# Kernel tuning notes

Hardware: AMD Instinct MI355X
Metric: run time of the kernel (lower is better)

The kernel has to match this reference:

```python
import jax, jax.numpy as jnp
import numpy as np

NP_ = 20000   # paper nodes
NA_ = 20000   # author nodes
E_AP = 400000
E_PP = 400000
D_IN, D_H, HEADS, D_HEAD, D_FF, D_OUT = 128, 256, 8, 32, 2048, 64


def setup_inputs() -> dict:
    key = jax.random.key(0)
    ks = iter(jax.random.split(key, 48))
    def nrm(shape, s=0.1):
        return jax.random.normal(next(ks), shape, jnp.float32) * s
    inp = {
        'feat_paper': nrm((NP_, D_IN), 1.0),
        'feat_author': nrm((NA_, D_IN), 1.0),
        'W_in_p': nrm((D_H, D_IN)), 'b_in_p': nrm((D_H,), 0.05),
        'W_in_a': nrm((D_H, D_IN)), 'b_in_a': nrm((D_H,), 0.05),
        'W_gat_ap': nrm((D_H, D_H)), 'al_ap': nrm((HEADS, D_HEAD)), 'ar_ap': nrm((HEADS, D_HEAD)), 'b_gat_ap': nrm((D_H,), 0.05),
        'W_gat_pp': nrm((D_H, D_H)), 'al_pp': nrm((HEADS, D_HEAD)), 'ar_pp': nrm((HEADS, D_HEAD)), 'b_gat_pp': nrm((D_H,), 0.05),
        'Wqkv_s': nrm((3 * D_H, D_H)), 'bqkv_s': nrm((3 * D_H,), 0.05), 'Wo_s': nrm((D_H, D_H)), 'bo_s': nrm((D_H,), 0.05),
        'Wqkv_c': nrm((3 * D_H, D_H)), 'bqkv_c': nrm((3 * D_H,), 0.05), 'Wo_c': nrm((D_H, D_H)), 'bo_c': nrm((D_H,), 0.05),
        'W_ff1': nrm((D_FF, D_H)), 'b_ff1': nrm((D_FF,), 0.05),
        'W_ff2': nrm((D_H, D_FF)), 'b_ff2': nrm((D_H,), 0.05),
        'ln1_g': jnp.ones((D_H,), jnp.float32), 'ln1_b': jnp.zeros((D_H,), jnp.float32),
        'ln2_g': jnp.ones((D_H,), jnp.float32), 'ln2_b': jnp.zeros((D_H,), jnp.float32),
        'ln3_g': jnp.ones((D_H,), jnp.float32), 'ln3_b': jnp.zeros((D_H,), jnp.float32),
        'W_pred': nrm((D_OUT, 3 * D_H)), 'b_pred': nrm((D_OUT,), 0.05),
        'ap_src': jax.random.randint(next(ks), (E_AP,), 0, NA_),
        'ap_dst': jax.random.randint(next(ks), (E_AP,), 0, NP_),
        'pp_src': jax.random.randint(next(ks), (E_PP,), 0, NP_),
        'pp_dst': jax.random.randint(next(ks), (E_PP,), 0, NP_),
    }
    return inp


def _leaky(x):
    return jnp.where(x > 0, x, 0.2 * x)  # DGL GATConv negative_slope=0.2


def _gat(x, src, dst, W, al, ar, b):
    """DGL GATConv on homogeneous graph with self-loops appended (eval mode)."""
    N = x.shape[0]
    h = (x @ W.T).reshape(N, HEADS, D_HEAD)          # fc has no bias in GATConv
    el = (h * al[None]).sum(-1)                      # (N, H)
    er = (h * ar[None]).sum(-1)                      # (N, H)
    sl = jnp.arange(N, dtype=src.dtype)              # self loops (add_self_loop)
    s = jnp.concatenate([src, sl])
    d = jnp.concatenate([dst, sl])
    e = _leaky(el[s] + er[d])                        # (E+N, H)
    m = jax.ops.segment_max(e, d, num_segments=N)    # edge-softmax per dst
    a = jnp.exp(e - m[d])
    z = jax.ops.segment_sum(a, d, num_segments=N)
    out = jax.ops.segment_sum(a[:, :, None] * h[s], d, num_segments=N)
    out = out / z[:, :, None] + b.reshape(1, HEADS, D_HEAD)
    return out.reshape(N, D_H)                       # flatten(start_dim=1)


def _ln(x, g, b):
    mu = x.mean(-1, keepdims=True)
    v = ((x - mu) ** 2).mean(-1, keepdims=True)
    return (x - mu) / jnp.sqrt(v + 1e-5) * g + b


def _mha(xq, xkv, Wqkv, bqkv, Wo, bo):
    Wq, Wk, Wv = jnp.split(Wqkv, 3, axis=0)
    bq, bk, bv = jnp.split(bqkv, 3)
    B, S, _ = xq.shape
    Sk = xkv.shape[1]
    q = (xq @ Wq.T + bq).reshape(B, S, HEADS, D_HEAD)
    k = (xkv @ Wk.T + bk).reshape(B, Sk, HEADS, D_HEAD)
    v = (xkv @ Wv.T + bv).reshape(B, Sk, HEADS, D_HEAD)
    att = jnp.einsum('bqhd,bkhd->bhqk', q, k) * (D_HEAD ** -0.5)
    a = jax.nn.softmax(att, axis=-1)
    o = jnp.einsum('bhqk,bkhd->bqhd', a, v).reshape(B, S, D_H)
    return o @ Wo.T + bo


def reference(feat_paper, feat_author, W_in_p, b_in_p, W_in_a, b_in_a,
              W_gat_ap, al_ap, ar_ap, b_gat_ap, W_gat_pp, al_pp, ar_pp, b_gat_pp,
              Wqkv_s, bqkv_s, Wo_s, bo_s, Wqkv_c, bqkv_c, Wo_c, bo_c,
              W_ff1, b_ff1, W_ff2, b_ff2, ln1_g, ln1_b, ln2_g, ln2_b, ln3_g, ln3_b,
              W_pred, b_pred, ap_src, ap_dst, pp_src, pp_dst):
    # fc_in per node type
    hp = feat_paper @ W_in_p.T + b_in_p              # (NP, D_H)
    ha = feat_author @ W_in_a.T + b_in_a             # (NA, D_H)
    Na = ha.shape[0]
    # etype 'ap': bipartite author->paper, to_homogeneous orders [author; paper]
    x_ap = jnp.concatenate([ha, hp], axis=0)
    out_ap = _gat(x_ap, ap_src, ap_dst + Na, W_gat_ap, al_ap, ar_ap, b_gat_ap)[Na:]
    # etype 'pp': paper->paper (single node set)
    out_pp = _gat(hp, pp_src, pp_dst, W_gat_pp, al_pp, ar_pp, b_gat_pp)
    # h dict order: 'paper', 'paper-author', 'paper-paper'
    tgt = jnp.stack([hp, out_ap, out_pp], axis=1)    # (NP, 3, D_H)
    # TransformerDecoderLayer (post-norm, relu, eval): memory = tgt
    x = _ln(tgt + _mha(tgt, tgt, Wqkv_s, bqkv_s, Wo_s, bo_s), ln1_g, ln1_b)
    x = _ln(x + _mha(x, tgt, Wqkv_c, bqkv_c, Wo_c, bo_c), ln2_g, ln2_b)
    ff = jax.nn.relu(x @ W_ff1.T + b_ff1) @ W_ff2.T + b_ff2
    z = _ln(x + ff, ln3_g, ln3_b)
    return z.reshape(z.shape[0], -1) @ W_pred.T + b_pred
```

## Files before the change

kernel.cpp:

```cpp
#include <hip/hip_runtime.h>
#include <hip/hip_bf16.h>
#include <cstdint>
#include <cstddef>

#define NP_N 20000
#define NA_N 20000
#define E_AP_N 400000
#define E_PP_N 400000

typedef __attribute__((ext_vector_type(8))) short bf16x8;
typedef __attribute__((ext_vector_type(4))) float f32x4;

__device__ __forceinline__ float b2f(ushort u) { return __uint_as_float(((uint32_t)u) << 16); }
__device__ __forceinline__ ushort f2b(float f) {
    uint32_t x = __float_as_uint(f);
    return (ushort)((x + 0x7fffu + ((x >> 16) & 1u)) >> 16);
}

#define LGKM_BARRIER() do { \
    asm volatile("s_waitcnt lgkmcnt(0)" ::: "memory"); \
    __builtin_amdgcn_s_barrier(); \
    __builtin_amdgcn_sched_barrier(0); \
} while (0)

#define NJOBS 14
struct PackJobs {
    const float* src[NJOBS];
    void* dst[NJOBS];
    int M[NJOBS], K[NJOBS];
    int type[NJOBS];
    int nquad[NJOBS];
    int blk0[NJOBS];
};

__global__ void pack_all_kernel(PackJobs J)
{
    int b = blockIdx.x;
    int j = 0;
    while (j + 1 < NJOBS && b >= J.blk0[j + 1]) ++j;
    int u = (b - J.blk0[j]) * 256 + threadIdx.x;
    if (u >= J.nquad[j]) return;
    int ty = J.type[j];
    const float* src = J.src[j];
    if (ty == 3) {
        float4 v = ((const float4*)src)[u];
        ushort4 o;
        o.x = f2b(v.x); o.y = f2b(v.y); o.z = f2b(v.z); o.w = f2b(v.w);
        ((ushort4*)J.dst[j])[u] = o;
    } else if (ty == 4) {
        int4 z = {0, 0, 0, 0};
        ((int4*)J.dst[j])[u] = z;
    } else if (ty == 0) {
        int M = J.M[j], K = J.K[j];
        int KT = K >> 5;
        int q = u & 1023;
        int jt = u >> 10;
        int t = jt % KT, jj = jt / KT;
        int ks = q >> 8, rem = q & 255;
        int r = rem >> 1;
        int e0 = (rem & 1) * 4;
        int row = jj * 128 + r;
        ushort4 o = {0, 0, 0, 0};
        if (row < M) {
            const float* s = src + (size_t)row * K + t * 32 + ks * 8 + e0;
            o.x = f2b(s[0]); o.y = f2b(s[1]); o.z = f2b(s[2]); o.w = f2b(s[3]);
        }
        ((ushort4*)J.dst[j])[u] = o;
    } else if (ty == 1) {
        int q = u & 2047, chunk = u >> 11;
        int s = q >> 6, rem = q & 63;
        int fl = rem >> 1, e0 = (rem & 1) * 4;
        const float* sp = src + (size_t)(chunk * 32 + fl) * 256 + s * 8 + e0;
        ushort4 o;
        o.x = f2b(sp[0]); o.y = f2b(sp[1]); o.z = f2b(sp[2]); o.w = f2b(sp[3]);
        ((ushort4*)J.dst[j])[u] = o;
    } else {
        int q = u & 2047, chunk = u >> 11;
        int s2 = q >> 9, rem = q & 511;
        int c = rem >> 1, e0 = (rem & 1) * 4;
        const float* sp = src + (size_t)c * 2048 + chunk * 32 + s2 * 8 + e0;
        ushort4 o;
        o.x = f2b(sp[0]); o.y = f2b(sp[1]); o.z = f2b(sp[2]); o.w = f2b(sp[3]);
        ((ushort4*)J.dst[j])[u] = o;
    }
}

template <int OUT_MODE>
__global__ __launch_bounds__(256) void gemm_mfma(
    const ushort* __restrict__ A, const ushort* __restrict__ Bp,
    const float* __restrict__ bias, void* __restrict__ Cv,
    int N, int M, int K, int lda)
{
    __shared__ __align__(16) ushort Ab[3][4096];
    __shared__ __align__(16) ushort Bb[3][4096];
    const int tid = threadIdx.x;
    const int lane = tid & 63;
    const int w = tid >> 6;
    const int wr = w >> 1, wc = w & 1;
    const int row0 = blockIdx.x * 128;
    const int col0 = blockIdx.y * 128;
    const int KT = K >> 5;
    const ushort* Bbase = Bp + (size_t)blockIdx.y * KT * 4096;
    f32x4 acc[4][4] = {};

    size_t aoff[2];
#pragma unroll
    for (int i = 0; i < 2; ++i) {
        int r = row0 + i * 64 + lane;
        if (r > N - 1) r = N - 1;
        aoff[i] = (size_t)r * lda + w * 8;
    }

    auto stage = [&](int buf, int t) {
        const int k0 = t << 5;
#pragma unroll
        for (int i = 0; i < 2; ++i) {
            __builtin_amdgcn_global_load_lds(
                (const __attribute__((address_space(1))) void*)(A + aoff[i] + k0),
                (__attribute__((address_space(3))) void*)(&Ab[buf][(w * 2 + i) * 512]), 16, 0, 0);
        }
#pragma unroll
        for (int i = 0; i < 2; ++i) {
            __builtin_amdgcn_global_load_lds(
                (const __attribute__((address_space(1))) void*)(Bbase + (size_t)t * 4096 + (w * 2 + i) * 512 + lane * 8),
                (__attribute__((address_space(3))) void*)(&Bb[buf][(w * 2 + i) * 512]), 16, 0, 0);
        }
    };

    stage(0, 0);
    stage(1, 1);

    int cur = 0;
    for (int t = 0; t < KT; ++t) {
        if (t + 1 < KT) { asm volatile("s_waitcnt vmcnt(4)" ::: "memory"); }
        else            { asm volatile("s_waitcnt vmcnt(0)" ::: "memory"); }
        __builtin_amdgcn_s_barrier();
        __builtin_amdgcn_sched_barrier(0);
        if (t + 2 < KT) {
            int nb = cur - 1; if (nb < 0) nb = 2;
            stage(nb, t + 2);
        }

        bf16x8 af[4], bfr[4];
        const int ks = lane >> 4;
        const int rl = lane & 15;
#pragma unroll
        for (int m = 0; m < 4; ++m)
            af[m] = *(const bf16x8*)&Ab[cur][ks * 1024 + (wr * 64 + m * 16 + rl) * 8];
#pragma unroll
        for (int n = 0; n < 4; ++n)
            bfr[n] = *(const bf16x8*)&Bb[cur][ks * 1024 + (wc * 64 + n * 16 + rl) * 8];
#pragma unroll
        for (int m = 0; m < 4; ++m)
#pragma unroll
            for (int n = 0; n < 4; ++n)
                acc[m][n] = __builtin_amdgcn_mfma_f32_16x16x32_bf16(af[m], bfr[n], acc[m][n], 0, 0, 0);

        cur = (cur == 2) ? 0 : cur + 1;
    }

#pragma unroll
    for (int m = 0; m < 4; ++m) {
#pragma unroll
        for (int n = 0; n < 4; ++n) {
            int gc = col0 + wc * 64 + n * 16 + (lane & 15);
            if (gc >= M) continue;
            float bv = bias ? bias[gc] : 0.f;
#pragma unroll
            for (int r = 0; r < 4; ++r) {
                int grow = row0 + wr * 64 + m * 16 + (lane >> 4) * 4 + r;
                if (grow >= N) continue;
                float v = acc[m][n][r] + bv;
                if (OUT_MODE == 2) v = fmaxf(v, 0.f);
                if (OUT_MODE == 1) ((float*)Cv)[(size_t)grow * M + gc] = v;
                else ((ushort*)Cv)[(size_t)grow * M + gc] = f2b(v);
            }
        }
    }
}

static inline void gemm_bf(const ushort* A, const ushort* Bp, const float* bias, void* C,
                           int N, int M, int K, int lda, int mode, hipStream_t s)
{
    dim3 g((N + 127) / 128, (M + 127) / 128);
    if (mode == 0)      gemm_mfma<0><<<g, 256, 0, s>>>(A, Bp, bias, C, N, M, K, lda);
    else if (mode == 1) gemm_mfma<1><<<g, 256, 0, s>>>(A, Bp, bias, C, N, M, K, lda);
    else                gemm_mfma<2><<<g, 256, 0, s>>>(A, Bp, bias, C, N, M, K, lda);
}

__global__ __launch_bounds__(256, 2) void ff_ln_kernel(
    const ushort* __restrict__ W1p, const ushort* __restrict__ W2p,
    const float* __restrict__ b1, const float* __restrict__ b2,
    const float* __restrict__ g3, const float* __restrict__ be3,
    ushort* X, int N)
{
    __shared__ __align__(16) ushort W1buf[8192];
    __shared__ __align__(16) ushort W2buf[8192];
    __shared__ __align__(16) ushort Sbuf[2048];
    const int tid = threadIdx.x;
    const int lane = tid & 63;
    const int w = tid >> 6;
    const int wr = w >> 1, wc = w & 1;
    const int row0 = blockIdx.x * 64;
    const int rl = lane & 15;
    const int ks = lane >> 4;

    bf16x8 xf[2][8];
#pragma unroll
    for (int m = 0; m < 2; ++m) {
        int gr = row0 + wr * 32 + m * 16 + rl;
        if (gr > N - 1) gr = N - 1;
        const ushort* xrow = X + (size_t)gr * 256 + ks * 8;
#pragma unroll
        for (int kc = 0; kc < 8; ++kc)
            xf[m][kc] = *(const bf16x8*)(xrow + kc * 32);
    }

    f32x4 oacc[2][8] = {};

    for (int fc = 0; fc < 64; ++fc) {
#pragma unroll
        for (int i = 0; i < 8; ++i) {
            int ii = w * 8 + i;
            const ushort* src;
            ushort* dst;
            if (ii < 16) {
                src = W1p + (size_t)fc * 8192 + ii * 512 + lane * 8;
                dst = &W1buf[ii * 512];
            } else {
                src = W2p + (size_t)fc * 8192 + (ii - 16) * 512 + lane * 8;
                dst = &W2buf[(ii - 16) * 512];
            }
            __builtin_amdgcn_global_load_lds(
                (const __attribute__((address_space(1))) void*)src,
                (__attribute__((address_space(3))) void*)dst, 16, 0, 0);
        }
        __syncthreads();

        f32x4 sacc[2] = {};
#pragma unroll
        for (int kc = 0; kc < 8; ++kc) {
            bf16x8 w1f = *(const bf16x8*)&W1buf[(kc * 4 + ks) * 256 + (wc * 16 + rl) * 8];
#pragma unroll
            for (int m = 0; m < 2; ++m)
                sacc[m] = __builtin_amdgcn_mfma_f32_16x16x32_bf16(w1f, xf[m][kc], sacc[m], 0, 0, 0);
        }
        {
            const int f0 = fc * 32;
            const int fb = wc * 16 + ks * 4;
            const int sidx = wc * 2 + (ks >> 1);
            const int e0 = (ks & 1) * 4;
            float4 b1v = *(const float4*)&b1[f0 + fb];
#pragma unroll
            for (int m = 0; m < 2; ++m) {
                ushort4 o;
                o.x = f2b(fmaxf(sacc[m][0] + b1v.x, 0.f));
                o.y = f2b(fmaxf(sacc[m][1] + b1v.y, 0.f));
                o.z = f2b(fmaxf(sacc[m][2] + b1v.z, 0.f));
                o.w = f2b(fmaxf(sacc[m][3] + b1v.w, 0.f));
                *(ushort4*)&Sbuf[(sidx * 64 + wr * 32 + m * 16 + rl) * 8 + e0] = o;
            }
        }
        LGKM_BARRIER();

        {
            bf16x8 sf[2];
#pragma unroll
            for (int m = 0; m < 2; ++m)
                sf[m] = *(const bf16x8*)&Sbuf[ks * 512 + (wr * 32 + m * 16 + rl) * 8];
#pragma unroll
            for (int n = 0; n < 8; ++n) {
                bf16x8 w2f = *(const bf16x8*)&W2buf[ks * 2048 + (wc * 128 + n * 16 + rl) * 8];
#pragma unroll
                for (int m = 0; m < 2; ++m)
                    oacc[m][n] = __builtin_amdgcn_mfma_f32_16x16x32_bf16(sf[m], w2f, oacc[m][n], 0, 0, 0);
            }
        }
        __syncthreads();
    }

    float2* lnb = (float2*)W1buf;
    float psum[2][4] = {}, psq[2][4] = {};
#pragma unroll
    for (int n = 0; n < 8; ++n) {
        int c = wc * 128 + n * 16 + rl;
        float bv = b2[c];
#pragma unroll
        for (int m = 0; m < 2; ++m)
#pragma unroll
            for (int r = 0; r < 4; ++r) {
                int grow = row0 + wr * 32 + m * 16 + ks * 4 + r;
                float v = oacc[m][n][r] + bv + b2f(X[(size_t)grow * 256 + c]);
                oacc[m][n][r] = v;
                psum[m][r] += v;
                psq[m][r] = fmaf(v, v, psq[m][r]);
            }
    }
#pragma unroll
    for (int off = 8; off >= 1; off >>= 1)
#pragma unroll
        for (int m = 0; m < 2; ++m)
#pragma unroll
            for (int r = 0; r < 4; ++r) {
                psum[m][r] += __shfl_xor(psum[m][r], off);
                psq[m][r]  += __shfl_xor(psq[m][r], off);
            }
    if (rl == 0) {
#pragma unroll
        for (int m = 0; m < 2; ++m)
#pragma unroll
            for (int r = 0; r < 4; ++r) {
                int lr = wr * 32 + m * 16 + ks * 4 + r;
                lnb[wc * 64 + lr] = make_float2(psum[m][r], psq[m][r]);
            }
    }
    __syncthreads();
    float mean_[2][4], rstd_[2][4];
#pragma unroll
    for (int m = 0; m < 2; ++m)
#pragma unroll
        for (int r = 0; r < 4; ++r) {
            int lr = wr * 32 + m * 16 + ks * 4 + r;
            float2 a0 = lnb[lr], a1 = lnb[64 + lr];
            float mean = (a0.x + a1.x) * (1.f / 256.f);
            float var = (a0.y + a1.y) * (1.f / 256.f) - mean * mean;
            mean_[m][r] = mean;
            rstd_[m][r] = rsqrtf(var + 1e-5f);
        }
#pragma unroll
    for (int n = 0; n < 8; ++n) {
        int c = wc * 128 + n * 16 + rl;
        float gv = g3[c], bev = be3[c];
#pragma unroll
        for (int m = 0; m < 2; ++m)
#pragma unroll
            for (int r = 0; r < 4; ++r) {
                int grow = row0 + wr * 32 + m * 16 + ks * 4 + r;
                if (grow < N)
                    X[(size_t)grow * 256 + c] =
                        f2b((oacc[m][n][r] - mean_[m][r]) * rstd_[m][r] * gv + bev);
            }
    }
}

__global__ void copy_col0_kernel(const ushort* __restrict__ src, ushort* __restrict__ tgt, int n)
{
    int i = blockIdx.x * blockDim.x + threadIdx.x;
    if (i >= n) return;
    int p = i >> 6, c = i & 63;
    ((ushort4*)tgt)[(size_t)p * 192 + c] = ((const ushort4*)src)[(size_t)p * 64 + c];
}

__global__ void attn_lr_all_kernel(
    const ushort* __restrict__ h0, const float* __restrict__ al0, const float* __restrict__ ar0,
    float* __restrict__ el0, float* __restrict__ er0,
    const ushort* __restrict__ h1, const float* __restrict__ al1, const float* __restrict__ ar1,
    float* __restrict__ el1, float* __restrict__ er1)
{
    int idx = blockIdx.x * blockDim.x + threadIdx.x;
    if (idx >= 480000) return;
    const ushort* h; const float *a1, *a2; float *el, *er; int i;
    if (idx < 320000) { h = h0; a1 = al0; a2 = ar0; el = el0; er = er0; i = idx; }
    else { h = h1; a1 = al1; a2 = ar1; el = el1; er = er1; i = idx - 320000; }
    int hd = i & 7;
    const ushort* hp = h + (size_t)(i >> 3) * 256 + hd * 32;
    const float* p1 = a1 + hd * 32;
    const float* p2 = a2 + hd * 32;
    float s1 = 0.f, s2 = 0.f;
#pragma unroll
    for (int j = 0; j < 8; ++j) {
        ushort4 t = ((const ushort4*)hp)[j];
        float v0 = b2f(t.x), v1 = b2f(t.y), v2 = b2f(t.z), v3 = b2f(t.w);
        s1 = fmaf(v0, p1[j * 4 + 0], s1); s2 = fmaf(v0, p2[j * 4 + 0], s2);
        s1 = fmaf(v1, p1[j * 4 + 1], s1); s2 = fmaf(v1, p2[j * 4 + 1], s2);
        s1 = fmaf(v2, p1[j * 4 + 2], s1); s2 = fmaf(v2, p2[j * 4 + 2], s2);
        s1 = fmaf(v3, p1[j * 4 + 3], s1); s2 = fmaf(v3, p2[j * 4 + 3], s2);
    }
    el[i] = s1;
    er[i] = s2;
}

__global__ void count2_kernel(const int* __restrict__ d0, int* __restrict__ c0,
                              const int* __restrict__ d1, int* __restrict__ c1, int E)
{
    int e = blockIdx.x * blockDim.x + threadIdx.x;
    if (e < E) atomicAdd(&c0[d0[e]], 1);
    else if (e < 2 * E) atomicAdd(&c1[d1[e - E]], 1);
}

__global__ void scan_chunk_kernel(const int* __restrict__ deg0, int* __restrict__ offs0,
                                  const int* __restrict__ deg1, int* __restrict__ offs1,
                                  int* __restrict__ parts, int N)
{
    int es = blockIdx.x / 20, ch = blockIdx.x % 20;
    const int* deg = es ? deg1 : deg0;
    int* offs = es ? offs1 : offs0;
    __shared__ int sbuf[1024];
    int tid = threadIdx.x;
    int i = ch * 1024 + tid;
    int v = (i < N) ? deg[i] : 0;
    sbuf[tid] = v;
    __syncthreads();
    for (int off = 1; off < 1024; off <<= 1) {
        int t = (tid >= off) ? sbuf[tid - off] : 0;
        __syncthreads();
        sbuf[tid] += t;
        __syncthreads();
    }
    if (i < N) offs[i] = sbuf[tid] - v;
    if (tid == 1023) parts[es * 21 + ch] = sbuf[1023];
}

__global__ void scan_parts_kernel(int* __restrict__ parts)
{
    int t = threadIdx.x;
    if ((t & 31) == 0 && t < 64) {
        int* p = parts + (t >> 5) * 21;
        int acc = 0;
#pragma unroll
        for (int i = 0; i < 20; ++i) { int x = p[i]; p[i] = acc; acc += x; }
        p[20] = acc;
    }
}

__global__ void scan_final_kernel(int* __restrict__ deg0, int* __restrict__ offs0,
                                  int* __restrict__ deg1, int* __restrict__ offs1,
                                  const int* __restrict__ parts, int N)
{
    int es = blockIdx.x / 20, ch = blockIdx.x % 20;
    int* deg = es ? deg1 : deg0;
    int* offs = es ? offs1 : offs0;
    int tid = threadIdx.x;
    int i = ch * 1024 + tid;
    if (i < N) { offs[i] += parts[es * 21 + ch]; deg[i] = 0; }
    if (ch == 19 && tid == 1023) offs[N] = parts[es * 21 + 20];
}

__global__ void scatter2_kernel(const int* __restrict__ s0, const int* __restrict__ d0,
                                const int* __restrict__ o0, int* __restrict__ c0, int* __restrict__ l0,
                                const int* __restrict__ s1, const int* __restrict__ d1,
                                const int* __restrict__ o1, int* __restrict__ c1, int* __restrict__ l1,
                                int E)
{
    int e = blockIdx.x * blockDim.x + threadIdx.x;
    if (e < E) {
        int d = d0[e];
        int pos = atomicAdd(&c0[d], 1);
        l0[o0[d] + pos] = s0[e];
    } else if (e < 2 * E) {
        int e1 = e - E;
        int d = d1[e1];
        int pos = atomicAdd(&c1[d], 1);
        l1[o1[d] + pos] = s1[e1];
    }
}

__global__ __launch_bounds__(64) void gat_agg_all_kernel(
    const ushort* __restrict__ ha, const float* __restrict__ ela, const float* __restrict__ era,
    const int* __restrict__ offsa, const int* __restrict__ lista, const float* __restrict__ biasa,
    const ushort* __restrict__ hp, const float* __restrict__ elp, const float* __restrict__ erp,
    const int* __restrict__ offsp, const int* __restrict__ listp, const float* __restrict__ biasp,
    ushort* __restrict__ out)
{
    int bid = blockIdx.x;
    const ushort* h; const float *el, *er, *bias; const int *offs, *elist;
    int p, dn, coloff;
    if (bid < NP_N) {
        h = ha; el = ela; er = era; offs = offsa; elist = lista; bias = biasa;
        p = bid; dn = NA_N + p; coloff = 256;
    } else {
        h = hp; el = elp; er = erp; offs = offsp; elist = listp; bias = biasp;
        p = bid - NP_N; dn = p; coloff = 512;
    }
    int l = threadIdx.x;
    int head = l >> 3;
    float erv = er[(size_t)dn * 8 + head];
    float acc[4] = {0.f, 0.f, 0.f, 0.f};
    float z = 0.f;
    int beg = offs[p], end = offs[p + 1];
    for (int e = beg - 1; e < end; ++e) {
        int s = (e < beg) ? dn : elist[e];
        float x = el[(size_t)s * 8 + head] + erv;
        x = x > 0.f ? x : 0.2f * x;
        float wgt = expf(x);
        z += wgt;
        ushort4 hv = *(const ushort4*)&h[(size_t)s * 256 + l * 4];
        acc[0] = fmaf(wgt, b2f(hv.x), acc[0]);
        acc[1] = fmaf(wgt, b2f(hv.y), acc[1]);
        acc[2] = fmaf(wgt, b2f(hv.z), acc[2]);
        acc[3] = fmaf(wgt, b2f(hv.w), acc[3]);
    }
    float inv = 1.f / z;
    ushort4 o;
    o.x = f2b(acc[0] * inv + bias[l * 4 + 0]);
    o.y = f2b(acc[1] * inv + bias[l * 4 + 1]);
    o.z = f2b(acc[2] * inv + bias[l * 4 + 2]);
    o.w = f2b(acc[3] * inv + bias[l * 4 + 3]);
    *(ushort4*)&out[(size_t)p * 768 + coloff + l * 4] = o;
}

__global__ void mha3_kernel(const ushort* qb, int ldq, int qoff,
                            const ushort* kvb, int ldkv, int koff, int voff,
                            ushort* ob, int ldo, int NPn)
{
    int idx = blockIdx.x * blockDim.x + threadIdx.x;
    if (idx >= NPn * 24) return;
    int h = idx & 7;
    int i = (idx >> 3) % 3;
    int p = idx / 24;
    float qr[32];
    {
        const ushort* q = qb + (size_t)(p * 3 + i) * ldq + qoff + h * 32;
#pragma unroll
        for (int j = 0; j < 8; ++j) {
            ushort4 t = ((const ushort4*)q)[j];
            qr[j * 4 + 0] = b2f(t.x); qr[j * 4 + 1] = b2f(t.y);
            qr[j * 4 + 2] = b2f(t.z); qr[j * 4 + 3] = b2f(t.w);
        }
    }
    float s[3];
#pragma unroll
    for (int j = 0; j < 3; ++j) {
        const ushort* k = kvb + (size_t)(p * 3 + j) * ldkv + koff + h * 32;
        float a = 0.f;
#pragma unroll
        for (int t4 = 0; t4 < 8; ++t4) {
            ushort4 t = ((const ushort4*)k)[t4];
            a = fmaf(qr[t4 * 4 + 0], b2f(t.x), a);
            a = fmaf(qr[t4 * 4 + 1], b2f(t.y), a);
            a = fmaf(qr[t4 * 4 + 2], b2f(t.z), a);
            a = fmaf(qr[t4 * 4 + 3], b2f(t.w), a);
        }
        s[j] = a * 0.17677669529663687f;
    }
    float m = fmaxf(s[0], fmaxf(s[1], s[2]));
    float e0 = expf(s[0] - m), e1 = expf(s[1] - m), e2 = expf(s[2] - m);
    float inv = 1.f / (e0 + e1 + e2);
    float aw[3] = {e0 * inv, e1 * inv, e2 * inv};
    float o[32] = {};
#pragma unroll
    for (int j = 0; j < 3; ++j) {
        const ushort* v = kvb + (size_t)(p * 3 + j) * ldkv + voff + h * 32;
#pragma unroll
        for (int t4 = 0; t4 < 8; ++t4) {
            ushort4 t = ((const ushort4*)v)[t4];
            o[t4 * 4 + 0] = fmaf(aw[j], b2f(t.x), o[t4 * 4 + 0]);
            o[t4 * 4 + 1] = fmaf(aw[j], b2f(t.y), o[t4 * 4 + 1]);
            o[t4 * 4 + 2] = fmaf(aw[j], b2f(t.z), o[t4 * 4 + 2]);
            o[t4 * 4 + 3] = fmaf(aw[j], b2f(t.w), o[t4 * 4 + 3]);
        }
    }
    ushort* op = ob + (size_t)(p * 3 + i) * ldo + h * 32;
#pragma unroll
    for (int t4 = 0; t4 < 8; ++t4) {
        ushort4 t;
        t.x = f2b(o[t4 * 4 + 0]); t.y = f2b(o[t4 * 4 + 1]);
        t.z = f2b(o[t4 * 4 + 2]); t.w = f2b(o[t4 * 4 + 3]);
        ((ushort4*)op)[t4] = t;
    }
}

__global__ __launch_bounds__(256) void add_ln_kernel(
    const ushort* __restrict__ a, const ushort* __restrict__ b,
    const float* __restrict__ g, const float* __restrict__ be,
    ushort* __restrict__ out, int rows)
{
    int row = blockIdx.x * 4 + (threadIdx.x >> 6);
    if (row >= rows) return;
    int l = threadIdx.x & 63;
    ushort4 va = *(const ushort4*)&a[(size_t)row * 256 + l * 4];
    ushort4 vb = *(const ushort4*)&b[(size_t)row * 256 + l * 4];
    float v[4];
    v[0] = b2f(va.x) + b2f(vb.x);
    v[1] = b2f(va.y) + b2f(vb.y);
    v[2] = b2f(va.z) + b2f(vb.z);
    v[3] = b2f(va.w) + b2f(vb.w);
    float s = v[0] + v[1] + v[2] + v[3];
#pragma unroll
    for (int off = 32; off; off >>= 1) s += __shfl_xor(s, off);
    float mean = s * (1.f / 256.f);
    float s2 = 0.f;
#pragma unroll
    for (int j = 0; j < 4; ++j) { float d = v[j] - mean; s2 = fmaf(d, d, s2); }
#pragma unroll
    for (int off = 32; off; off >>= 1) s2 += __shfl_xor(s2, off);
    float rstd = rsqrtf(s2 * (1.f / 256.f) + 1e-5f);
    ushort4 o;
    o.x = f2b((v[0] - mean) * rstd * g[l * 4 + 0] + be[l * 4 + 0]);
    o.y = f2b((v[1] - mean) * rstd * g[l * 4 + 1] + be[l * 4 + 1]);
    o.z = f2b((v[2] - mean) * rstd * g[l * 4 + 2] + be[l * 4 + 2]);
    o.w = f2b((v[3] - mean) * rstd * g[l * 4 + 3] + be[l * 4 + 3]);
    *(ushort4*)&out[(size_t)row * 256 + l * 4] = o;
}

extern "C" void kernel_launch(void* const* d_in, const int* in_sizes, int n_in,
                              void* d_out, int out_size, void* d_ws, size_t ws_size,
                              hipStream_t stream)
{
    const float* feat_paper  = (const float*)d_in[0];
    const float* feat_author = (const float*)d_in[1];
    const float* W_in_p  = (const float*)d_in[2];
    const float* b_in_p  = (const float*)d_in[3];
    const float* W_in_a  = (const float*)d_in[4];
    const float* b_in_a  = (const float*)d_in[5];
    const float* W_gat_ap = (const float*)d_in[6];
    const float* al_ap    = (const float*)d_in[7];
    const float* ar_ap    = (const float*)d_in[8];
    const float* b_gat_ap = (const float*)d_in[9];
    const float* W_gat_pp = (const float*)d_in[10];
    const float* al_pp    = (const float*)d_in[11];
    const float* ar_pp    = (const float*)d_in[12];
    const float* b_gat_pp = (const float*)d_in[13];
    const float* Wqkv_s = (const float*)d_in[14];
    const float* bqkv_s = (const float*)d_in[15];
    const float* Wo_s   = (const float*)d_in[16];
    const float* bo_s   = (const float*)d_in[17];
    const float* Wqkv_c = (const float*)d_in[18];
    const float* bqkv_c = (const float*)d_in[19];
    const float* Wo_c   = (const float*)d_in[20];
    const float* bo_c   = (const float*)d_in[21];
    const float* W_ff1  = (const float*)d_in[22];
    const float* b_ff1  = (const float*)d_in[23];
    const float* W_ff2  = (const float*)d_in[24];
    const float* b_ff2  = (const float*)d_in[25];
    const float* ln1_g  = (const float*)d_in[26];
    const float* ln1_b  = (const float*)d_in[27];
    const float* ln2_g  = (const float*)d_in[28];
    const float* ln2_b  = (const float*)d_in[29];
    const float* ln3_g  = (const float*)d_in[30];
    const float* ln3_b  = (const float*)d_in[31];
    const float* W_pred = (const float*)d_in[32];
    const float* b_pred = (const float*)d_in[33];
    const int* ap_src = (const int*)d_in[34];
    const int* ap_dst = (const int*)d_in[35];
    const int* pp_src = (const int*)d_in[36];
    const int* pp_dst = (const int*)d_in[37];

    const int NP = NP_N, NA = NA_N;

    uint8_t* wsb = (uint8_t*)d_ws;
    ushort* tgt_bf = (ushort*)wsb;
    ushort* X_bf   = (ushort*)(wsb + 30720000);
    ushort* WB     = (ushort*)(wsb + 61440000);
    ushort* p_in_p   = WB + 0;
    ushort* p_in_a   = WB + 32768;
    ushort* p_gat_ap = WB + 65536;
    ushort* p_gat_pp = WB + 131072;
    ushort* p_qkv_s  = WB + 196608;
    ushort* p_o_s    = WB + 393216;
    ushort* p_qkv_c  = WB + 458752;
    ushort* p_o_c    = WB + 655360;
    ushort* p_pred   = WB + 720896;
    ushort* p_ff1    = WB + 819200;
    ushort* p_ff2    = WB + 1343488;
    uint8_t* BIG = wsb + 65280000;

    ushort* feat_p_bf = (ushort*)BIG;
    ushort* feat_a_bf = (ushort*)(BIG + 5120000);
    ushort* x_ap_bf   = (ushort*)(BIG + 10240000);
    ushort* hp_bf     = x_ap_bf + (size_t)NA * 256;
    ushort* h_ap_bf   = (ushort*)(BIG + 30720000);
    ushort* h_pp_bf   = (ushort*)(BIG + 51200000);
    float* el_ap = (float*)(BIG + 61440000);
    float* er_ap = (float*)(BIG + 62720000);
    float* el_pp = (float*)(BIG + 64000000);
    float* er_pp = (float*)(BIG + 64640000);
    int* ireg    = (int*)(BIG + 65280000);
    int* ap_offs = ireg;
    int* pp_offs = ireg + 20004;
    int* ap_cur  = ireg + 40008;
    int* pp_cur  = ireg + 60008;
    int* ap_list = ireg + 80008;
    int* pp_list = ireg + 480008;
    int* parts   = ireg + 880008;

    {
        PackJobs J;
        const float* srcs[NJOBS] = { feat_paper, feat_author, W_in_p, W_in_a, W_gat_ap,
                                     W_gat_pp, Wqkv_s, Wo_s, Wqkv_c, Wo_c, W_pred,
                                     W_ff1, W_ff2, nullptr };
        void* dsts[NJOBS] = { feat_p_bf, feat_a_bf, p_in_p, p_in_a, p_gat_ap,
                              p_gat_pp, p_qkv_s, p_o_s, p_qkv_c, p_o_c, p_pred,
                              p_ff1, p_ff2, ap_cur };
        int Ms[NJOBS]  = {0,0, 256,256,256,256, 768,256,768,256, 64, 0,0, 0};
        int Ks[NJOBS]  = {0,0, 128,128,256,256, 256,256,256,256, 768, 0,0, 0};
        int tys[NJOBS] = {3,3, 0,0,0,0, 0,0,0,0, 0, 1,2, 4};
        int nq[NJOBS]  = {640000,640000, 8192,8192,16384,16384, 49152,16384,49152,16384,
                          24576, 131072,131072, 10000};
        int acc = 0;
        for (int j = 0; j < NJOBS; ++j) {
            J.src[j] = srcs[j]; J.dst[j] = dsts[j];
            J.M[j] = Ms[j]; J.K[j] = Ks[j]; J.type[j] = tys[j]; J.nquad[j] = nq[j];
            J.blk0[j] = acc;
            acc += (nq[j] + 255) / 256;
        }
        pack_all_kernel<<<acc, 256, 0, stream>>>(J);
    }

    gemm_bf(feat_a_bf, p_in_a, b_in_a, x_ap_bf, NA, 256, 128, 128, 0, stream);
    gemm_bf(feat_p_bf, p_in_p, b_in_p, hp_bf,   NP, 256, 128, 128, 0, stream);

    copy_col0_kernel<<<(NP * 64 + 255) / 256, 256, 0, stream>>>(hp_bf, tgt_bf, NP * 64);

    gemm_bf(x_ap_bf, p_gat_ap, nullptr, h_ap_bf, NA + NP, 256, 256, 256, 0, stream);
    gemm_bf(hp_bf,   p_gat_pp, nullptr, h_pp_bf, NP,      256, 256, 256, 0, stream);

    attn_lr_all_kernel<<<1875, 256, 0, stream>>>(h_ap_bf, al_ap, ar_ap, el_ap, er_ap,
                                                 h_pp_bf, al_pp, ar_pp, el_pp, er_pp);

    count2_kernel<<<3125, 256, 0, stream>>>(ap_dst, ap_cur, pp_dst, pp_cur, E_AP_N);
    scan_chunk_kernel<<<40, 1024, 0, stream>>>(ap_cur, ap_offs, pp_cur, pp_offs, parts, NP);
    scan_parts_kernel<<<1, 64, 0, stream>>>(parts);
    scan_final_kernel<<<40, 1024, 0, stream>>>(ap_cur, ap_offs, pp_cur, pp_offs, parts, NP);
    scatter2_kernel<<<3125, 256, 0, stream>>>(ap_src, ap_dst, ap_offs, ap_cur, ap_list,
                                              pp_src, pp_dst, pp_offs, pp_cur, pp_list, E_AP_N);

    gat_agg_all_kernel<<<2 * NP, 64, 0, stream>>>(
        h_ap_bf, el_ap, er_ap, ap_offs, ap_list, b_gat_ap,
        h_pp_bf, el_pp, er_pp, pp_offs, pp_list, b_gat_pp, tgt_bf);

    {
        ushort* qkv = (ushort*)BIG;
        gemm_bf(tgt_bf, p_qkv_s, bqkv_s, qkv, 60000, 768, 256, 256, 0, stream);
        mha3_kernel<<<(NP * 24 + 255) / 256, 256, 0, stream>>>(qkv, 768, 0, qkv, 768, 256, 512, qkv, 768, NP);
        gemm_bf(qkv, p_o_s, bo_s, X_bf, 60000, 256, 256, 768, 0, stream);
        add_ln_kernel<<<15000, 256, 0, stream>>>(tgt_bf, X_bf, ln1_g, ln1_b, X_bf, 60000);
    }

    {
        ushort* qb  = (ushort*)BIG;
        ushort* kvb = (ushort*)(BIG + 30720000);
        const ushort* p_kv_c = p_qkv_c + (size_t)2 * 8 * 4096;
        gemm_bf(X_bf,   p_qkv_c, bqkv_c,       qb,  60000, 256, 256, 256, 0, stream);
        gemm_bf(tgt_bf, p_kv_c,  bqkv_c + 256, kvb, 60000, 512, 256, 256, 0, stream);
        mha3_kernel<<<(NP * 24 + 255) / 256, 256, 0, stream>>>(qb, 256, 0, kvb, 512, 0, 256, qb, 256, NP);
        gemm_bf(qb, p_o_c, bo_c, kvb, 60000, 256, 256, 256, 0, stream);
        add_ln_kernel<<<15000, 256, 0, stream>>>(X_bf, kvb, ln2_g, ln2_b, X_bf, 60000);
    }

    ff_ln_kernel<<<(60000 + 63) / 64, 256, 0, stream>>>(p_ff1, p_ff2, b_ff1, b_ff2,
                                                        ln3_g, ln3_b, X_bf, 60000);

    gemm_bf(X_bf, p_pred, b_pred, (float*)d_out, NP, 64, 768, 768, 1, stream);
}
```

Measured before the change: 805.3 us.

## Fuse attention output projection with residual add and LayerNorm

Adds a proj_ln_kernel that computes the attention output projection with MFMA on 64-row tiles, then adds the bias and residual and applies LayerNorm before writing. It replaces the separate GEMM plus add_ln_kernel in both the self- and cross-attention blocks. This removes one kernel launch per block and the round trip of the projection output through global memory. In exchange every block reloads the full 256x256 weight from L2. Variance is now computed as E[x^2]-mean^2, which is slightly less numerically robust.

```diff
diff --git a/kernel.cpp b/kernel.cpp
--- a/kernel.cpp
+++ b/kernel.cpp
@@ -188,6 +188,120 @@
     else                gemm_mfma<2><<<g, 256, 0, s>>>(A, Bp, bias, C, N, M, K, lda);
 }
 
+__global__ __launch_bounds__(256, 2) void proj_ln_kernel(
+    const ushort* o, int ldo,
+    const ushort* __restrict__ Bp, const float* __restrict__ bo,
+    const ushort* res, int ldr,
+    const float* __restrict__ g, const float* __restrict__ be,
+    ushort* X, int N)
+{
+    __shared__ __align__(16) ushort Wb[8192];
+    const int tid = threadIdx.x;
+    const int lane = tid & 63;
+    const int w = tid >> 6;
+    const int wr = w >> 1, wc = w & 1;
+    const int row0 = blockIdx.x * 64;
+    const int rl = lane & 15;
+    const int ks = lane >> 4;
+
+    int arow[2];
+#pragma unroll
+    for (int m = 0; m < 2; ++m) {
+        int r = row0 + wr * 32 + m * 16 + rl;
+        arow[m] = (r < N) ? r : (N - 1);
+    }
+
+    f32x4 oacc[2][8] = {};
+
+    for (int t = 0; t < 8; ++t) {
+#pragma unroll
+        for (int i = 0; i < 4; ++i) {
+            int ii = w * 4 + i;
+            const ushort* src = Bp + ((size_t)(ii >> 3) * 8 + t) * 4096 + (ii & 7) * 512 + lane * 8;
+            __builtin_amdgcn_global_load_lds(
+                (const __attribute__((address_space(1))) void*)src,
+                (__attribute__((address_space(3))) void*)(&Wb[ii * 512]), 16, 0, 0);
+        }
+        bf16x8 af[2];
+#pragma unroll
+        for (int m = 0; m < 2; ++m)
+            af[m] = *(const bf16x8*)(o + (size_t)arow[m] * ldo + t * 32 + ks * 8);
+        __syncthreads();
+
+#pragma unroll
+        for (int n = 0; n < 8; ++n) {
+            bf16x8 bfr = *(const bf16x8*)&Wb[wc * 4096 + ks * 1024 + (n * 16 + rl) * 8];
+#pragma unroll
+            for (int m = 0; m < 2; ++m)
+                oacc[m][n] = __builtin_amdgcn_mfma_f32_16x16x32_bf16(af[m], bfr, oacc[m][n], 0, 0, 0);
+        }
+        __syncthreads();
+    }
+
+    float2* lnb = (float2*)Wb;
+    float psum[2][4] = {}, psq[2][4] = {};
+#pragma unroll
+    for (int n = 0; n < 8; ++n) {
+        int c = wc * 128 + n * 16 + rl;
+        float bv = bo[c];
+#pragma unroll
+        for (int m = 0; m < 2; ++m)
+#pragma unroll
+            for (int r = 0; r < 4; ++r) {
+                int grow = row0 + wr * 32 + m * 16 + ks * 4 + r;
+                float v = oacc[m][n][r] + bv + b2f(res[(size_t)grow * ldr + c]);
+                oacc[m][n][r] = v;
+                psum[m][r] += v;
+                psq[m][r] = fmaf(v, v, psq[m][r]);
+            }
+    }
+#pragma unroll
+    for (int off = 8; off >= 1; off >>= 1)
+#pragma unroll
+        for (int m = 0; m < 2; ++m)
+#pragma unroll
+            for (int r = 0; r < 4; ++r) {
+                psum[m][r] += __shfl_xor(psum[m][r], off);
+                psq[m][r]  += __shfl_xor(psq[m][r], off);
+            }
+    if (rl == 0) {
+#pragma unroll
+        for (int m = 0; m < 2; ++m)
+#pragma unroll
+            for (int r = 0; r < 4; ++r) {
+                int lr = wr * 32 + m * 16 + ks * 4 + r;
+                lnb[wc * 64 + lr] = make_float2(psum[m][r], psq[m][r]);
+            }
+    }
+    __syncthreads();
+    float mean_[2][4], rstd_[2][4];
+#pragma unroll
+    for (int m = 0; m < 2; ++m)
+#pragma unroll
+        for (int r = 0; r < 4; ++r) {
+            int lr = wr * 32 + m * 16 + ks * 4 + r;
+            float2 a0 = lnb[lr], a1 = lnb[64 + lr];
+            float mean = (a0.x + a1.x) * (1.f / 256.f);
+            float var = (a0.y + a1.y) * (1.f / 256.f) - mean * mean;
+            mean_[m][r] = mean;
+            rstd_[m][r] = rsqrtf(var + 1e-5f);
+        }
+#pragma unroll
+    for (int n = 0; n < 8; ++n) {
+        int c = wc * 128 + n * 16 + rl;
+        float gv = g[c], bev = be[c];
+#pragma unroll
+        for (int m = 0; m < 2; ++m)
+#pragma unroll
+            for (int r = 0; r < 4; ++r) {
+                int grow = row0 + wr * 32 + m * 16 + ks * 4 + r;
+                if (grow < N)
+                    X[(size_t)grow * 256 + c] =
+                        f2b((oacc[m][n][r] - mean_[m][r]) * rstd_[m][r] * gv + bev);
+            }
+    }
+}
+
 __global__ __launch_bounds__(256, 2) void ff_ln_kernel(
     const ushort* __restrict__ W1p, const ushort* __restrict__ W2p,
     const float* __restrict__ b1, const float* __restrict__ b2,
@@ -558,39 +672,6 @@
         t.z = f2b(o[t4 * 4 + 2]); t.w = f2b(o[t4 * 4 + 3]);
         ((ushort4*)op)[t4] = t;
     }
-}
-
-__global__ __launch_bounds__(256) void add_ln_kernel(
-    const ushort* __restrict__ a, const ushort* __restrict__ b,
-    const float* __restrict__ g, const float* __restrict__ be,
-    ushort* __restrict__ out, int rows)
-{
-    int row = blockIdx.x * 4 + (threadIdx.x >> 6);
-    if (row >= rows) return;
-    int l = threadIdx.x & 63;
-    ushort4 va = *(const ushort4*)&a[(size_t)row * 256 + l * 4];
-    ushort4 vb = *(const ushort4*)&b[(size_t)row * 256 + l * 4];
-    float v[4];
-    v[0] = b2f(va.x) + b2f(vb.x);
-    v[1] = b2f(va.y) + b2f(vb.y);
-    v[2] = b2f(va.z) + b2f(vb.z);
-    v[3] = b2f(va.w) + b2f(vb.w);
-    float s = v[0] + v[1] + v[2] + v[3];
-#pragma unroll
-    for (int off = 32; off; off >>= 1) s += __shfl_xor(s, off);
-    float mean = s * (1.f / 256.f);
-    float s2 = 0.f;
-#pragma unroll
-    for (int j = 0; j < 4; ++j) { float d = v[j] - mean; s2 = fmaf(d, d, s2); }
-#pragma unroll
-    for (int off = 32; off; off >>= 1) s2 += __shfl_xor(s2, off);
-    float rstd = rsqrtf(s2 * (1.f / 256.f) + 1e-5f);
-    ushort4 o;
-    o.x = f2b((v[0] - mean) * rstd * g[l * 4 + 0] + be[l * 4 + 0]);
-    o.y = f2b((v[1] - mean) * rstd * g[l * 4 + 1] + be[l * 4 + 1]);
-    o.z = f2b((v[2] - mean) * rstd * g[l * 4 + 2] + be[l * 4 + 2]);
-    o.w = f2b((v[3] - mean) * rstd * g[l * 4 + 3] + be[l * 4 + 3]);
-    *(ushort4*)&out[(size_t)row * 256 + l * 4] = o;
 }
 
 extern "C" void kernel_launch(void* const* d_in, const int* in_sizes, int n_in,
@@ -723,8 +804,8 @@
         ushort* qkv = (ushort*)BIG;
         gemm_bf(tgt_bf, p_qkv_s, bqkv_s, qkv, 60000, 768, 256, 256, 0, stream);
         mha3_kernel<<<(NP * 24 + 255) / 256, 256, 0, stream>>>(qkv, 768, 0, qkv, 768, 256, 512, qkv, 768, NP);
-        gemm_bf(qkv, p_o_s, bo_s, X_bf, 60000, 256, 256, 768, 0, stream);
-        add_ln_kernel<<<15000, 256, 0, stream>>>(tgt_bf, X_bf, ln1_g, ln1_b, X_bf, 60000);
+        proj_ln_kernel<<<(60000 + 63) / 64, 256, 0, stream>>>(
+            qkv, 768, p_o_s, bo_s, tgt_bf, 256, ln1_g, ln1_b, X_bf, 60000);
     }
 
     {
@@ -734,8 +815,8 @@
         gemm_bf(X_bf,   p_qkv_c, bqkv_c,       qb,  60000, 256, 256, 256, 0, stream);
         gemm_bf(tgt_bf, p_kv_c,  bqkv_c + 256, kvb, 60000, 512, 256, 256, 0, stream);
         mha3_kernel<<<(NP * 24 + 255) / 256, 256, 0, stream>>>(qb, 256, 0, kvb, 512, 0, 256, qb, 256, NP);
-        gemm_bf(qb, p_o_c, bo_c, kvb, 60000, 256, 256, 256, 0, stream);
-        add_ln_kernel<<<15000, 256, 0, stream>>>(X_bf, kvb, ln2_g, ln2_b, X_bf, 60000);
+        proj_ln_kernel<<<(60000 + 63) / 64, 256, 0, stream>>>(
+            qb, 256, p_o_c, bo_c, X_bf, 256, ln2_g, ln2_b, X_bf, 60000);
     }
 
     ff_ln_kernel<<<(60000 + 63) / 64, 256, 0, stream>>>(p_ff1, p_ff2, b_ff1, b_ff2,
```

Result: faster. 778.8 us (-3.3%).
